# Performance work log

Hardware: AMD Instinct MI355X
Metric: run time of the kernel (lower is better)

The kernel has to match this reference:

```python
import jax, jax.numpy as jnp
import numpy as np


def _forward(agent_qs, ally_states, enemy_states, W_al, b_al, W_en, b_en, Wq, bq, Wk, bk,
             w1_W1, w1_b1, w1_W2, w1_b2, wf_W1, wf_b1, wf_W2, wf_b2, hb_W, hb_b,
             v_W1, v_b1, v_W2, v_b2):
    A, B, S, _ = ally_states.shape
    E = A + enemy_states.shape[0]
    D = W_al.shape[1]
    Da = Wq.shape[1]
    # entity encoders: [A,B,S,D], [En,B,S,D]
    ally_embed = ally_states @ W_al + b_al
    enemy_embed = enemy_states @ W_en + b_en
    entity = jnp.concatenate([ally_embed, enemy_embed], axis=0)      # [E,B,S,D]
    ent_bs = jnp.transpose(entity, (1, 2, 0, 3))                     # [B,S,E,D]
    q = ent_bs @ Wq + bq                                             # [B,S,E,Da]
    k = ent_bs @ Wk + bk                                             # [B,S,E,Da]
    scale = jnp.asarray(Da, q.dtype) ** 0.5
    energy = jnp.einsum('bsid,bsjd->bsij', q / scale, k)             # [B,S,E,E]
    # torch softmax(dim=1) on [BS,E,E] == softmax over the query axis i
    attn = jax.nn.softmax(energy, axis=2)
    # bmm(value[BS,D,E], attn).mean(-1) == value @ mean_j attn[:, :, e, j]
    attn_mean = jnp.mean(attn, axis=3)                               # [B,S,E]
    attn_out = jnp.einsum('bsed,bse->bsd', ent_bs, attn_mean)        # [B,S,D]
    ally_bs = jnp.transpose(ally_embed, (1, 2, 0, 3))                # [B,S,A,D]
    emi = jnp.concatenate(
        [jnp.broadcast_to(attn_out[:, :, None, :], (B, S, A, D)), ally_bs], axis=-1)  # [B,S,A,2D]
    # hypernets (2-layer)
    w1 = jnp.abs(jax.nn.relu(emi @ w1_W1 + w1_b1) @ w1_W2 + w1_b2)   # [B,S,A,M]
    b1 = attn_out @ hb_W + hb_b                                      # [B,S,M]
    hidden = jax.nn.elu(jnp.einsum('bsa,bsam->bsm', agent_qs, w1) + b1)
    wf = jnp.abs(jax.nn.relu(attn_out @ wf_W1 + wf_b1) @ wf_W2 + wf_b2)  # [B,S,M]
    v = jax.nn.relu(attn_out @ v_W1 + v_b1) @ v_W2 + v_b2            # [B,S,1]
    q_tot = jnp.einsum('bsm,bsm->bs', hidden, wf)[..., None] + v     # [B,S,1]
    return q_tot


def setup_inputs() -> dict:
    key = jax.random.key(0)
    B, S, A, En = 128, 128, 8, 8
    NFal, NFen, D, Da, M, H = 32, 16, 64, 128, 32, 64
    ks = jax.random.split(key, 32)
    p = lambda i, shape: jax.random.normal(ks[i], shape, dtype=jnp.float32) * 0.05
    return dict(
        agent_qs=jax.random.normal(ks[0], (B, S, A), dtype=jnp.float32),
        ally_states=jax.random.normal(ks[1], (A, B, S, NFal), dtype=jnp.float32),
        enemy_states=jax.random.normal(ks[2], (En, B, S, NFen), dtype=jnp.float32),
        W_al=p(3, (NFal, D)), b_al=p(4, (D,)), W_en=p(5, (NFen, D)), b_en=p(6, (D,)),
        Wq=p(7, (D, Da)), bq=p(8, (Da,)), Wk=p(9, (D, Da)), bk=p(10, (Da,)),
        w1_W1=p(11, (2 * D, H)), w1_b1=p(12, (H,)), w1_W2=p(13, (H, M)), w1_b2=p(14, (M,)),
        wf_W1=p(15, (D, H)), wf_b1=p(16, (H,)), wf_W2=p(17, (H, M)), wf_b2=p(18, (M,)),
        hb_W=p(19, (D, M)), hb_b=p(20, (M,)),
        v_W1=p(21, (D, M)), v_b1=p(22, (M,)), v_W2=p(23, (M, 1)), v_b2=p(24, (1,)),
    )


def reference(agent_qs, ally_states, enemy_states, W_al, b_al, W_en, b_en, Wq, bq, Wk, bk,
              w1_W1, w1_b1, w1_W2, w1_b2, wf_W1, wf_b1, wf_W2, wf_b2, hb_W, hb_b,
              v_W1, v_b1, v_W2, v_b2):
    return _forward(agent_qs, ally_states, enemy_states, W_al, b_al, W_en, b_en, Wq, bq, Wk, bk,
                    w1_W1, w1_b1, w1_W2, w1_b2, wf_W1, wf_b1, wf_W2, wf_b2, hb_W, hb_b,
                    v_W1, v_b1, v_W2, v_b2)
```

## Files before the change

kernel.cpp:

```cpp
#include <hip/hip_runtime.h>
#include <hip/hip_bf16.h>


#define B_   128
#define S_   128
#define BS_  (B_ * S_)
#define INV_S 0.08838834764831845f

typedef short bs8 __attribute__((ext_vector_type(8)));
typedef float f4  __attribute__((ext_vector_type(4)));

#define MFMA(a, b, c) __builtin_amdgcn_mfma_f32_16x16x32_bf16((a), (b), (c), 0, 0, 0)
#define LOADB(t) (*(const bs8*)&fb[(size_t)(t) * 512 + lane * 8])

__device__ __forceinline__ short f2bf(float f) {
    union { float f; unsigned u; } v; v.f = f;
    unsigned r = v.u + 0x7fffu + ((v.u >> 16) & 1u);
    return (short)(r >> 16);
}

__global__ __launch_bounds__(64)
void qmix_pre1(const float* __restrict__ Wq, const float* __restrict__ Wk,
               const float* __restrict__ bk,
               float* __restrict__ Ms, float* __restrict__ vq)
{
    const int blk = blockIdx.x, t = threadIdx.x;
    float p;
    if (blk < 4096) {
        const int k = blk >> 6, n = blk & 63;
        p = Wq[k * 128 + t] * Wk[n * 128 + t]
          + Wq[k * 128 + 64 + t] * Wk[n * 128 + 64 + t];
        #pragma unroll
        for (int off = 32; off >= 1; off >>= 1) p += __shfl_down(p, off, 64);
        if (t == 0) Ms[k * 64 + n] = p * INV_S;
    } else {
        const int d = blk - 4096;
        p = Wq[d * 128 + t] * bk[t] + Wq[d * 128 + 64 + t] * bk[64 + t];
        #pragma unroll
        for (int off = 32; off >= 1; off >>= 1) p += __shfl_down(p, off, 64);
        if (t == 0) vq[d] = p * INV_S;
    }
}

__global__ __launch_bounds__(64)
void qmix_pack(const float* __restrict__ Ms,
               const float* __restrict__ W_al, const float* __restrict__ W_en,
               const float* __restrict__ w1_W1, const float* __restrict__ w1_W2,
               const float* __restrict__ vq,
               const float* __restrict__ wf_W1, const float* __restrict__ hb_W,
               const float* __restrict__ v_W1,  const float* __restrict__ wf_W2,
               short* __restrict__ fb)
{
    const int blk = blockIdx.x, lane = threadIdx.x;
    const int quad = lane >> 4, l16 = lane & 15;
    bs8 v;
    if (blk < 8) {
        const int ks = blk >> 2, n = (blk & 3) * 16 + l16;
        #pragma unroll
        for (int j = 0; j < 8; ++j)
            v[j] = f2bf(Ms[(ks * 32 + quad * 8 + j) * 64 + n]);
    } else if (blk < 16) {
        const bool en = (blk >= 12);
        const float* W = en ? W_en : W_al;
        const int Krows = en ? 16 : 32;
        const int n = ((blk - (en ? 12 : 8)) & 3) * 16 + l16;
        #pragma unroll
        for (int j = 0; j < 8; ++j) {
            const int k = quad * 8 + j;
            v[j] = (k < Krows) ? f2bf(W[k * 64 + n]) : (short)0;
        }
    } else if (blk < 32) {
        const int t = blk - 16, ks = t >> 2, n = (t & 3) * 16 + l16;
        #pragma unroll
        for (int j = 0; j < 8; ++j)
            v[j] = f2bf(w1_W1[(ks * 32 + quad * 8 + j) * 64 + n]);
    } else if (blk < 36) {
        const int t = blk - 32, ks = t >> 1, n = (t & 1) * 16 + l16;
        #pragma unroll
        for (int j = 0; j < 8; ++j)
            v[j] = f2bf(w1_W2[(ks * 32 + quad * 8 + j) * 32 + n]);
    } else if (blk < 38) {
        const int ks = blk - 36;
        #pragma unroll
        for (int j = 0; j < 8; ++j)
            v[j] = (l16 == 0) ? f2bf(vq[ks * 32 + quad * 8 + j]) : (short)0;
    } else if (blk < 54) {
        const int t = blk - 38, ks = t >> 3, n = (t & 7) * 16 + l16;
        #pragma unroll
        for (int j = 0; j < 8; ++j) {
            const int k = ks * 32 + quad * 8 + j;
            float w;
            if (n < 64)       w = wf_W1[k * 64 + n];
            else if (n < 96)  w = hb_W[k * 32 + (n - 64)];
            else              w = v_W1[k * 32 + (n - 96)];
            v[j] = f2bf(w);
        }
    } else {
        const int t = blk - 54, ks = t >> 1, n = (t & 1) * 16 + l16;
        #pragma unroll
        for (int j = 0; j < 8; ++j)
            v[j] = f2bf(wf_W2[(ks * 32 + quad * 8 + j) * 32 + n]);
    }
    *(bs8*)&fb[(size_t)blk * 512 + lane * 8] = v;
}

struct __align__(16) WaveLds {
    short ent[2][16][72];
    short aoutb[2][64];
    short hb16[2][64];
    float qs[2][8];
};

__global__ __launch_bounds__(128, 4)
void qmix_main(const float* __restrict__ agent_qs,
               const float* __restrict__ ally, const float* __restrict__ enemy,
               const float* __restrict__ b_al, const float* __restrict__ b_en,
               const float* __restrict__ w1_b1, const float* __restrict__ w1_b2,
               const float* __restrict__ wf_b1, const float* __restrict__ wf_b2,
               const float* __restrict__ hb_b,  const float* __restrict__ v_b1,
               const float* __restrict__ v_W2,  const float* __restrict__ v_b2,
               const short* __restrict__ fb,
               float* __restrict__ out)
{
    const int w    = threadIdx.x >> 6;
    const int lane = threadIdx.x & 63;
    const int quad = lane >> 4, l16 = lane & 15;
    const int half = lane >> 5;
    const int qh   = quad & 1;
    const int siteA = blockIdx.x * 4 + w * 2;

    __shared__ WaveLds lds[2];
    WaveLds& L = lds[w];

    if (lane < 16)
        L.qs[lane >> 3][lane & 7] =
            agent_qs[(size_t)(siteA + (lane >> 3)) * 8 + (lane & 7)];

    f4 encf[2][4];
    #pragma unroll
    for (int s = 0; s < 2; ++s) {
        const int site = siteA + s;
        bs8 a_al = {0,0,0,0,0,0,0,0}, a_en = {0,0,0,0,0,0,0,0};
        if (l16 < 8) {
            const float* pa = ally + ((size_t)l16 * BS_ + site) * 32 + quad * 8;
            const float4 f0 = *(const float4*)pa, f1 = *(const float4*)(pa + 4);
            a_al[0]=f2bf(f0.x); a_al[1]=f2bf(f0.y); a_al[2]=f2bf(f0.z); a_al[3]=f2bf(f0.w);
            a_al[4]=f2bf(f1.x); a_al[5]=f2bf(f1.y); a_al[6]=f2bf(f1.z); a_al[7]=f2bf(f1.w);
        } else if (quad < 2) {
            const float* pe = enemy + ((size_t)(l16 - 8) * BS_ + site) * 16 + quad * 8;
            const float4 f0 = *(const float4*)pe, f1 = *(const float4*)(pe + 4);
            a_en[0]=f2bf(f0.x); a_en[1]=f2bf(f0.y); a_en[2]=f2bf(f0.z); a_en[3]=f2bf(f0.w);
            a_en[4]=f2bf(f1.x); a_en[5]=f2bf(f1.y); a_en[6]=f2bf(f1.z); a_en[7]=f2bf(f1.w);
        }
        #pragma unroll
        for (int n0t = 0; n0t < 4; ++n0t) {
            f4 acc = {0.f, 0.f, 0.f, 0.f};
            acc = MFMA(a_al, LOADB(8 + n0t), acc);
            acc = MFMA(a_en, LOADB(12 + n0t), acc);
            const int d = n0t * 16 + l16;
            const float bal = b_al[d], ben = b_en[d];
            #pragma unroll
            for (int r = 0; r < 4; ++r) {
                const int row = quad * 4 + r;
                const float v = acc[r] + (row < 8 ? bal : ben);
                encf[s][n0t][r] = v;
                L.ent[s][row][d] = f2bf(v);
            }
        }
    }
    __syncthreads();

    bs8 ae0s[2], ae1s[2];
    #pragma unroll
    for (int s = 0; s < 2; ++s) {
        ae0s[s] = *(const bs8*)&L.ent[s][l16][quad * 8];
        ae1s[s] = *(const bs8*)&L.ent[s][l16][32 + quad * 8];
    }
    const short (*entP)[72] = (l16 < 8) ? L.ent[0] : L.ent[1];
    const bs8 ag0 = *(const bs8*)&entP[l16 & 7][quad * 8];
    const bs8 ag1 = *(const bs8*)&entP[l16 & 7][32 + quad * 8];
    __syncthreads();

    f4 pqs[2];
    #pragma unroll
    for (int s = 0; s < 2; ++s) {
        f4 pq = {0.f, 0.f, 0.f, 0.f};
        pq = MFMA(ae0s[s], LOADB(36), pq);
        pq = MFMA(ae1s[s], LOADB(37), pq);
        pqs[s] = pq;
        #pragma unroll
        for (int n0t = 0; n0t < 4; ++n0t) {
            f4 acc = {0.f, 0.f, 0.f, 0.f};
            acc = MFMA(ae0s[s], LOADB(0 + n0t), acc);
            acc = MFMA(ae1s[s], LOADB(4 + n0t), acc);
            const int d = n0t * 16 + l16;
            #pragma unroll
            for (int r = 0; r < 4; ++r) L.ent[s][quad * 4 + r][d] = f2bf(acc[r]);
        }
    }
    __syncthreads();

    #pragma unroll
    for (int s = 0; s < 2; ++s) {
        f4 eacc = {0.f, 0.f, 0.f, 0.f};
        {
            const bs8 at0 = *(const bs8*)&L.ent[s][l16][quad * 8];
            const bs8 at1 = *(const bs8*)&L.ent[s][l16][32 + quad * 8];
            eacc = MFMA(at0, ae0s[s], eacc);
            eacc = MFMA(at1, ae1s[s], eacc);
            const int src = lane & 48;
            #pragma unroll
            for (int r = 0; r < 4; ++r) eacc[r] += __shfl(pqs[s][r], src, 64);
        }
        float cmax = fmaxf(fmaxf(eacc[0], eacc[1]), fmaxf(eacc[2], eacc[3]));
        cmax = fmaxf(cmax, __shfl_xor(cmax, 16, 64));
        cmax = fmaxf(cmax, __shfl_xor(cmax, 32, 64));
        float er[4], csum = 0.f;
        #pragma unroll
        for (int r = 0; r < 4; ++r) { er[r] = __expf(eacc[r] - cmax); csum += er[r]; }
        csum += __shfl_xor(csum, 16, 64);
        csum += __shfl_xor(csum, 32, 64);
        const float inv = 1.f / csum;
        float amean[4];
        #pragma unroll
        for (int r = 0; r < 4; ++r) {
            float p = er[r] * inv;
            p += __shfl_xor(p, 1, 64);
            p += __shfl_xor(p, 2, 64);
            p += __shfl_xor(p, 4, 64);
            p += __shfl_xor(p, 8, 64);
            amean[r] = p * (1.f / 16.f);
        }
        #pragma unroll
        for (int n0t = 0; n0t < 4; ++n0t) {
            float ap = amean[0] * encf[s][n0t][0] + amean[1] * encf[s][n0t][1]
                     + amean[2] * encf[s][n0t][2] + amean[3] * encf[s][n0t][3];
            ap += __shfl_xor(ap, 16, 64);
            ap += __shfl_xor(ap, 32, 64);
            if (quad == 0) L.aoutb[s][n0t * 16 + l16] = f2bf(ap);
        }
    }
    __syncthreads();

    const short* aoP = L.aoutb[l16 >> 3];
    const bs8 aab0 = *(const bs8*)&aoP[quad * 8];
    const bs8 aab1 = *(const bs8*)&aoP[32 + quad * 8];

    float xm[8];
    #pragma unroll
    for (int n0t = 0; n0t < 8; ++n0t) {
        f4 acc = {0.f, 0.f, 0.f, 0.f};
        acc = MFMA(aab0, LOADB(38 + n0t), acc);
        acc = MFMA(aab1, LOADB(46 + n0t), acc);
        xm[n0t] = acc[0];
    }
    #pragma unroll
    for (int n0t = 0; n0t < 4; ++n0t) {
        const int t = n0t * 16 + l16;
        L.hb16[half][t] = f2bf(fmaxf(xm[n0t] + wf_b1[t], 0.f));
    }
    const int m32 = lane & 31;
    const float b1m = xm[4 + qh] + hb_b[m32];
    float vsum;
    {
        float hv = fmaxf(xm[6 + qh] + v_b1[m32], 0.f) * v_W2[m32];
        hv += __shfl_xor(hv, 1, 64);
        hv += __shfl_xor(hv, 2, 64);
        hv += __shfl_xor(hv, 4, 64);
        hv += __shfl_xor(hv, 8, 64);
        hv += __shfl_xor(hv, 16, 64);
        vsum = hv;
    }
    __syncthreads();

    float wfm;
    {
        const short* hfP = L.hb16[l16 >> 3];
        const bs8 hf0 = *(const bs8*)&hfP[quad * 8];
        const bs8 hf1 = *(const bs8*)&hfP[32 + quad * 8];
        f4 acc0 = {0.f, 0.f, 0.f, 0.f};
        acc0 = MFMA(hf0, LOADB(54), acc0);
        acc0 = MFMA(hf1, LOADB(56), acc0);
        f4 acc1 = {0.f, 0.f, 0.f, 0.f};
        acc1 = MFMA(hf0, LOADB(55), acc1);
        acc1 = MFMA(hf1, LOADB(57), acc1);
        wfm = fabsf((qh ? acc1[0] : acc0[0]) + wf_b2[m32]);
    }

    #pragma unroll
    for (int n0t = 0; n0t < 4; ++n0t) {
        f4 acc = {0.f, 0.f, 0.f, 0.f};
        acc = MFMA(aab0, LOADB(16 + 0 + n0t), acc);
        acc = MFMA(aab1, LOADB(16 + 4 + n0t), acc);
        acc = MFMA(ag0,  LOADB(16 + 8 + n0t), acc);
        acc = MFMA(ag1,  LOADB(16 + 12 + n0t), acc);
        const int d = n0t * 16 + l16;
        const float b1v = w1_b1[d];
        #pragma unroll
        for (int r = 0; r < 4; ++r)
            L.ent[0][quad * 4 + r][d] = f2bf(fmaxf(acc[r] + b1v, 0.f));
    }
    __syncthreads();

    float pm;
    {
        const bs8 ha0 = *(const bs8*)&L.ent[0][l16][quad * 8];
        const bs8 ha1 = *(const bs8*)&L.ent[0][l16][32 + quad * 8];
        const float* qsv = L.qs[half];
        float p0 = 0.f, p1 = 0.f;
        #pragma unroll
        for (int n0t = 0; n0t < 2; ++n0t) {
            f4 acc = {0.f, 0.f, 0.f, 0.f};
            acc = MFMA(ha0, LOADB(32 + 0 + n0t), acc);
            acc = MFMA(ha1, LOADB(32 + 2 + n0t), acc);
            const float b2v = w1_b2[n0t * 16 + l16];
            float p = 0.f;
            #pragma unroll
            for (int r = 0; r < 4; ++r)
                p += qsv[qh * 4 + r] * fabsf(acc[r] + b2v);
            if (n0t == 0) p0 = p; else p1 = p;
        }
        p0 += __shfl_xor(p0, 16, 64);
        p1 += __shfl_xor(p1, 16, 64);
        pm = qh ? p1 : p0;
    }

    float hp = pm + b1m;
    hp = (hp > 0.f) ? hp : (__expf(hp) - 1.f);
    float contrib = hp * wfm;
    contrib += __shfl_xor(contrib, 1, 64);
    contrib += __shfl_xor(contrib, 2, 64);
    contrib += __shfl_xor(contrib, 4, 64);
    contrib += __shfl_xor(contrib, 8, 64);
    contrib += __shfl_xor(contrib, 16, 64);
    if ((lane & 31) == 0)
        out[siteA + half] = contrib + vsum + v_b2[0];
}

extern "C" void kernel_launch(void* const* d_in, const int* in_sizes, int n_in,
                              void* d_out, int out_size, void* d_ws, size_t ws_size,
                              hipStream_t stream) {
    const float* p[25];
    for (int i = 0; i < 25; ++i) p[i] = (const float*)d_in[i];
    short* fb = (short*)d_ws;
    float* vq = (float*)((char*)d_ws + 58 * 512 * 2);
    float* Ms = vq + 64;

    qmix_pre1<<<4096 + 64, 64, 0, stream>>>(p[7], p[9], p[10], Ms, vq);
    qmix_pack<<<58, 64, 0, stream>>>(Ms, p[3], p[5], p[11], p[13], vq,
                                     p[15], p[19], p[21], p[17], fb);
    qmix_main<<<BS_ / 4, 128, 0, stream>>>(
        p[0], p[1], p[2], p[4], p[6], p[12], p[14],
        p[16], p[18], p[20], p[22], p[23], p[24],
        fb, (float*)d_out);
}
```

Measured before the change: 155.0 us.

## Fold Wq·Wk precompute into pack kernel and drop fp32 entity registers

Removes the separate qmix_pre1 launch by having the pack kernel compute the Wq·Wk^T and Wq·bk products directly before bf16 packing, which saves one kernel launch and an intermediate global buffer. In the main kernel, the fp32 encoder outputs (encf) are no longer held in registers. The attention-weighted sum now reads bf16 entity values back from LDS, and a new scratch LDS region keeps the entity tile alive so a sync and early loads can go. This cuts register pressure and one barrier, at the cost of more LDS per block and slightly lower precision in the attention sum. The pack blocks that do the dot products are serial and may become a longer critical path.

```diff
diff --git a/kernel.cpp b/kernel.cpp
--- a/kernel.cpp
+++ b/kernel.cpp
@@ -18,35 +18,17 @@
     unsigned r = v.u + 0x7fffu + ((v.u >> 16) & 1u);
     return (short)(r >> 16);
 }
+__device__ __forceinline__ float bf2f(short s) {
+    union { unsigned u; float f; } v;
+    v.u = ((unsigned)(unsigned short)s) << 16;
+    return v.f;
+}
 
 __global__ __launch_bounds__(64)
-void qmix_pre1(const float* __restrict__ Wq, const float* __restrict__ Wk,
+void qmix_pack(const float* __restrict__ Wq,   const float* __restrict__ Wk,
                const float* __restrict__ bk,
-               float* __restrict__ Ms, float* __restrict__ vq)
-{
-    const int blk = blockIdx.x, t = threadIdx.x;
-    float p;
-    if (blk < 4096) {
-        const int k = blk >> 6, n = blk & 63;
-        p = Wq[k * 128 + t] * Wk[n * 128 + t]
-          + Wq[k * 128 + 64 + t] * Wk[n * 128 + 64 + t];
-        #pragma unroll
-        for (int off = 32; off >= 1; off >>= 1) p += __shfl_down(p, off, 64);
-        if (t == 0) Ms[k * 64 + n] = p * INV_S;
-    } else {
-        const int d = blk - 4096;
-        p = Wq[d * 128 + t] * bk[t] + Wq[d * 128 + 64 + t] * bk[64 + t];
-        #pragma unroll
-        for (int off = 32; off >= 1; off >>= 1) p += __shfl_down(p, off, 64);
-        if (t == 0) vq[d] = p * INV_S;
-    }
-}
-
-__global__ __launch_bounds__(64)
-void qmix_pack(const float* __restrict__ Ms,
                const float* __restrict__ W_al, const float* __restrict__ W_en,
                const float* __restrict__ w1_W1, const float* __restrict__ w1_W2,
-               const float* __restrict__ vq,
                const float* __restrict__ wf_W1, const float* __restrict__ hb_W,
                const float* __restrict__ v_W1,  const float* __restrict__ wf_W2,
                short* __restrict__ fb)
@@ -56,9 +38,18 @@
     bs8 v;
     if (blk < 8) {
         const int ks = blk >> 2, n = (blk & 3) * 16 + l16;
-        #pragma unroll
-        for (int j = 0; j < 8; ++j)
-            v[j] = f2bf(Ms[(ks * 32 + quad * 8 + j) * 64 + n]);
+        float acc[8] = {0.f,0.f,0.f,0.f,0.f,0.f,0.f,0.f};
+        const float4* wk4 = (const float4*)(Wk + n * 128);
+        for (int t4 = 0; t4 < 32; ++t4) {
+            const float4 wk = wk4[t4];
+            #pragma unroll
+            for (int j = 0; j < 8; ++j) {
+                const float4 wq = *(const float4*)(Wq + (ks * 32 + quad * 8 + j) * 128 + t4 * 4);
+                acc[j] += wq.x * wk.x + wq.y * wk.y + wq.z * wk.z + wq.w * wk.w;
+            }
+        }
+        #pragma unroll
+        for (int j = 0; j < 8; ++j) v[j] = f2bf(acc[j] * INV_S);
     } else if (blk < 16) {
         const bool en = (blk >= 12);
         const float* W = en ? W_en : W_al;
@@ -81,9 +72,19 @@
             v[j] = f2bf(w1_W2[(ks * 32 + quad * 8 + j) * 32 + n]);
     } else if (blk < 38) {
         const int ks = blk - 36;
+        float acc[8] = {0.f,0.f,0.f,0.f,0.f,0.f,0.f,0.f};
+        const float4* bk4 = (const float4*)bk;
+        for (int t4 = 0; t4 < 32; ++t4) {
+            const float4 b = bk4[t4];
+            #pragma unroll
+            for (int j = 0; j < 8; ++j) {
+                const float4 wq = *(const float4*)(Wq + (ks * 32 + quad * 8 + j) * 128 + t4 * 4);
+                acc[j] += wq.x * b.x + wq.y * b.y + wq.z * b.z + wq.w * b.w;
+            }
+        }
         #pragma unroll
         for (int j = 0; j < 8; ++j)
-            v[j] = (l16 == 0) ? f2bf(vq[ks * 32 + quad * 8 + j]) : (short)0;
+            v[j] = (l16 == 0) ? f2bf(acc[j] * INV_S) : (short)0;
     } else if (blk < 54) {
         const int t = blk - 38, ks = t >> 3, n = (t & 7) * 16 + l16;
         #pragma unroll
@@ -106,6 +107,7 @@
 
 struct __align__(16) WaveLds {
     short ent[2][16][72];
+    short scr[2][16][72];
     short aoutb[2][64];
     short hb16[2][64];
     float qs[2][8];
@@ -136,7 +138,6 @@
         L.qs[lane >> 3][lane & 7] =
             agent_qs[(size_t)(siteA + (lane >> 3)) * 8 + (lane & 7)];
 
-    f4 encf[2][4];
     #pragma unroll
     for (int s = 0; s < 2; ++s) {
         const int site = siteA + s;
@@ -162,9 +163,7 @@
             #pragma unroll
             for (int r = 0; r < 4; ++r) {
                 const int row = quad * 4 + r;
-                const float v = acc[r] + (row < 8 ? bal : ben);
-                encf[s][n0t][r] = v;
-                L.ent[s][row][d] = f2bf(v);
+                L.ent[s][row][d] = f2bf(acc[r] + (row < 8 ? bal : ben));
             }
         }
     }
@@ -176,10 +175,6 @@
         ae0s[s] = *(const bs8*)&L.ent[s][l16][quad * 8];
         ae1s[s] = *(const bs8*)&L.ent[s][l16][32 + quad * 8];
     }
-    const short (*entP)[72] = (l16 < 8) ? L.ent[0] : L.ent[1];
-    const bs8 ag0 = *(const bs8*)&entP[l16 & 7][quad * 8];
-    const bs8 ag1 = *(const bs8*)&entP[l16 & 7][32 + quad * 8];
-    __syncthreads();
 
     f4 pqs[2];
     #pragma unroll
@@ -195,7 +190,7 @@
             acc = MFMA(ae1s[s], LOADB(4 + n0t), acc);
             const int d = n0t * 16 + l16;
             #pragma unroll
-            for (int r = 0; r < 4; ++r) L.ent[s][quad * 4 + r][d] = f2bf(acc[r]);
+            for (int r = 0; r < 4; ++r) L.scr[s][quad * 4 + r][d] = f2bf(acc[r]);
         }
     }
     __syncthreads();
@@ -204,8 +199,8 @@
     for (int s = 0; s < 2; ++s) {
         f4 eacc = {0.f, 0.f, 0.f, 0.f};
         {
-            const bs8 at0 = *(const bs8*)&L.ent[s][l16][quad * 8];
-            const bs8 at1 = *(const bs8*)&L.ent[s][l16][32 + quad * 8];
+            const bs8 at0 = *(const bs8*)&L.scr[s][l16][quad * 8];
+            const bs8 at1 = *(const bs8*)&L.scr[s][l16][32 + quad * 8];
             eacc = MFMA(at0, ae0s[s], eacc);
             eacc = MFMA(at1, ae1s[s], eacc);
             const int src = lane & 48;
@@ -233,11 +228,14 @@
         }
         #pragma unroll
         for (int n0t = 0; n0t < 4; ++n0t) {
-            float ap = amean[0] * encf[s][n0t][0] + amean[1] * encf[s][n0t][1]
-                     + amean[2] * encf[s][n0t][2] + amean[3] * encf[s][n0t][3];
+            const int d = n0t * 16 + l16;
+            float ap = amean[0] * bf2f(L.ent[s][quad * 4 + 0][d])
+                     + amean[1] * bf2f(L.ent[s][quad * 4 + 1][d])
+                     + amean[2] * bf2f(L.ent[s][quad * 4 + 2][d])
+                     + amean[3] * bf2f(L.ent[s][quad * 4 + 3][d]);
             ap += __shfl_xor(ap, 16, 64);
             ap += __shfl_xor(ap, 32, 64);
-            if (quad == 0) L.aoutb[s][n0t * 16 + l16] = f2bf(ap);
+            if (quad == 0) L.aoutb[s][d] = f2bf(ap);
         }
     }
     __syncthreads();
@@ -287,25 +285,30 @@
         wfm = fabsf((qh ? acc1[0] : acc0[0]) + wf_b2[m32]);
     }
 
-    #pragma unroll
-    for (int n0t = 0; n0t < 4; ++n0t) {
-        f4 acc = {0.f, 0.f, 0.f, 0.f};
-        acc = MFMA(aab0, LOADB(16 + 0 + n0t), acc);
-        acc = MFMA(aab1, LOADB(16 + 4 + n0t), acc);
-        acc = MFMA(ag0,  LOADB(16 + 8 + n0t), acc);
-        acc = MFMA(ag1,  LOADB(16 + 12 + n0t), acc);
-        const int d = n0t * 16 + l16;
-        const float b1v = w1_b1[d];
-        #pragma unroll
-        for (int r = 0; r < 4; ++r)
-            L.ent[0][quad * 4 + r][d] = f2bf(fmaxf(acc[r] + b1v, 0.f));
+    {
+        const short (*entP)[72] = (l16 < 8) ? L.ent[0] : L.ent[1];
+        const bs8 ag0 = *(const bs8*)&entP[l16 & 7][quad * 8];
+        const bs8 ag1 = *(const bs8*)&entP[l16 & 7][32 + quad * 8];
+        #pragma unroll
+        for (int n0t = 0; n0t < 4; ++n0t) {
+            f4 acc = {0.f, 0.f, 0.f, 0.f};
+            acc = MFMA(aab0, LOADB(16 + 0 + n0t), acc);
+            acc = MFMA(aab1, LOADB(16 + 4 + n0t), acc);
+            acc = MFMA(ag0,  LOADB(16 + 8 + n0t), acc);
+            acc = MFMA(ag1,  LOADB(16 + 12 + n0t), acc);
+            const int d = n0t * 16 + l16;
+            const float b1v = w1_b1[d];
+            #pragma unroll
+            for (int r = 0; r < 4; ++r)
+                L.scr[0][quad * 4 + r][d] = f2bf(fmaxf(acc[r] + b1v, 0.f));
+        }
     }
     __syncthreads();
 
     float pm;
     {
-        const bs8 ha0 = *(const bs8*)&L.ent[0][l16][quad * 8];
-        const bs8 ha1 = *(const bs8*)&L.ent[0][l16][32 + quad * 8];
+        const bs8 ha0 = *(const bs8*)&L.scr[0][l16][quad * 8];
+        const bs8 ha1 = *(const bs8*)&L.scr[0][l16][32 + quad * 8];
         const float* qsv = L.qs[half];
         float p0 = 0.f, p1 = 0.f;
         #pragma unroll
@@ -343,12 +346,9 @@
     const float* p[25];
     for (int i = 0; i < 25; ++i) p[i] = (const float*)d_in[i];
     short* fb = (short*)d_ws;
-    float* vq = (float*)((char*)d_ws + 58 * 512 * 2);
-    float* Ms = vq + 64;
-
-    qmix_pre1<<<4096 + 64, 64, 0, stream>>>(p[7], p[9], p[10], Ms, vq);
-    qmix_pack<<<58, 64, 0, stream>>>(Ms, p[3], p[5], p[11], p[13], vq,
-                                     p[15], p[19], p[21], p[17], fb);
+
+    qmix_pack<<<58, 64, 0, stream>>>(p[7], p[9], p[10], p[3], p[5],
+                                     p[11], p[13], p[15], p[19], p[21], p[17], fb);
     qmix_main<<<BS_ / 4, 128, 0, stream>>>(
         p[0], p[1], p[2], p[4], p[6], p[12], p[14],
         p[16], p[18], p[20], p[22], p[23], p[24],
```

Result: no change. 153.2 us (-1.2%).
